# Optimization experiments

Hardware: AMD Instinct MI355X
Metric: run time of the kernel (lower is better)

Reference implementation:

```python
import jax, jax.numpy as jnp
import numpy as np

N, DEG, F_IN, H = 50000, 16, 128, 32
E = N * DEG


def _linear_params(key, out_f, in_f):
    kw, kb = jax.random.split(key)
    s = 1.0 / np.sqrt(in_f)
    W = jax.random.uniform(kw, (out_f, in_f), jnp.float32, -s, s)
    b = jax.random.uniform(kb, (out_f,), jnp.float32, -s, s)
    return W, b


def setup_inputs() -> dict:
    key = jax.random.key(0)
    ks = jax.random.split(key, 12)
    X = jax.random.normal(ks[0], (N, F_IN), jnp.float32)
    # DEG distinct nonzero offsets shared by all rows -> unique (src,dst) pairs,
    # so the COO tensor is already coalesced (no duplicate indices).
    offsets = jax.random.permutation(ks[1], jnp.arange(1, N))[:DEG]
    src = jnp.repeat(jnp.arange(N, dtype=jnp.int32), DEG)
    dst = ((src.reshape(N, DEG) + offsets[None, :].astype(jnp.int32)) % N).reshape(-1)
    D = jax.ops.segment_sum(jnp.ones((E,), jnp.float32), src, num_segments=N)
    wn1p, bn1p = _linear_params(ks[2], H, F_IN)      # convN1.pass_map
    wn1s, bn1s = _linear_params(ks[3], H, F_IN)      # convN1.self_map
    we1p, be1p = _linear_params(ks[4], H, 2 * H)     # convE1.pass_map
    we1s, be1s = _linear_params(ks[5], H, F_IN)      # convE1.self_map
    wn2p, bn2p = _linear_params(ks[6], H, H)         # convN2.pass_map
    wn2s, bn2s = _linear_params(ks[7], H, H)         # convN2.self_map
    we2p, be2p = _linear_params(ks[8], H, 2 * H)     # convE2.pass_map
    we2s, be2s = _linear_params(ks[9], H, H)         # convE2.self_map
    wc, bc = _linear_params(ks[10], 1, H)            # classifier
    return dict(X=X, src=src, dst=dst, D=D,
                wn1p=wn1p, bn1p=bn1p, wn1s=wn1s, bn1s=bn1s,
                we1p=we1p, be1p=be1p, we1s=we1s, be1s=be1s,
                wn2p=wn2p, bn2p=bn2p, wn2s=wn2s, bn2s=bn2s,
                we2p=we2p, be2p=be2p, we2s=we2s, be2s=be2s,
                wc=wc, bc=bc)


def reference(X, src, dst, D,
              wn1p, bn1p, wn1s, bn1s,
              we1p, be1p, we1s, be1s,
              wn2p, bn2p, wn2s, bn2s,
              we2p, be2p, we2s, be2s,
              wc, bc):
    n = X.shape[0]

    def node_conv(vals, Xn, wp, bp, ws, bs):
        # torch.sparse.sum(A, dim=1): sum edge values per source row
        Asum = jax.ops.segment_sum(vals, src, num_segments=n)
        return jax.nn.relu((Asum / D[:, None]) @ wp.T + bp + Xn @ ws.T + bs)

    def edge_conv(vals, Xn, wp, bp, ws, bs):
        X1, X2 = Xn[src], Xn[dst]
        Ef = jnp.concatenate([(X1 - X2) * 0.5, (X1 + X2) * 0.5], axis=-1)
        return jax.nn.relu(Ef @ wp.T + bp + vals @ ws.T + bs)

    # add_graph: edge features = |X[src] - X[dst]|
    vals0 = jnp.abs(X[src] - X[dst])            # (E, F_IN)
    X0 = jnp.zeros_like(X)                       # forward zeros node features
    Xn1 = node_conv(vals0, X0, wn1p, bn1p, wn1s, bn1s)   # (N, 32)
    vals1 = edge_conv(vals0, Xn1, we1p, be1p, we1s, be1s)  # (E, 32)
    Xn2 = node_conv(vals1, Xn1, wn2p, bn2p, wn2s, bn2s)  # (N, 32)
    vals2 = edge_conv(vals1, Xn2, we2p, be2p, we2s, be2s)  # (E, 32)
    SX = jax.nn.sigmoid(vals2 @ wc.T + bc)[:, 0]          # (E,)
    return SX
```

## Files before the change

kernel.cpp:

```cpp
#include <hip/hip_runtime.h>

#define DEG 16
#define F_IN 128
#define H 32
#define CH 16

typedef __attribute__((ext_vector_type(8))) _Float16 f16x8;
typedef __attribute__((ext_vector_type(4))) float f32x4;
typedef __attribute__((ext_vector_type(4))) int i32x4;

union HS { _Float16 f; unsigned short s; };

__device__ __forceinline__ float relu_f(float x) { return fmaxf(x, 0.0f); }

__device__ __forceinline__ f16x8 habs8(f16x8 a) {
    union { f16x8 h; i32x4 i; } u; u.h = a;
#pragma unroll
    for (int k = 0; k < 4; ++k) u.i[k] &= 0x7FFF7FFF;
    return u.h;
}
__device__ __forceinline__ unsigned short f2h_s(float x) {
    HS v; v.f = (_Float16)x; return v.s;
}

__global__ __launch_bounds__(256) void k_xhalf(
    const float* __restrict__ X, _Float16* __restrict__ Xh, long n8)
{
    const long t = (long)blockIdx.x * 256 + threadIdx.x;
    if (t >= n8) return;
    const float4* p = (const float4*)X + t * 2;
    const float4 a = p[0], b = p[1];
    f16x8 h;
    h[0] = (_Float16)a.x; h[1] = (_Float16)a.y; h[2] = (_Float16)a.z; h[3] = (_Float16)a.w;
    h[4] = (_Float16)b.x; h[5] = (_Float16)b.y; h[6] = (_Float16)b.z; h[7] = (_Float16)b.w;
    *(f16x8*)(Xh + t * 8) = h;
}

__global__ __launch_bounds__(256) void k_prep(
    const float* __restrict__ we1s, const float* __restrict__ we1p,
    const float* __restrict__ be1p, const float* __restrict__ be1s,
    const float* __restrict__ we2p, const float* __restrict__ we2s,
    const float* __restrict__ be2p, const float* __restrict__ be2s,
    const float* __restrict__ wn1p, const float* __restrict__ bn1p,
    const float* __restrict__ bn1s,
    const float* __restrict__ wn2p, const float* __restrict__ bn2p,
    const float* __restrict__ wn2s, const float* __restrict__ bn2s,
    _Float16* __restrict__ Wcat1, _Float16* __restrict__ Wcat2,
    _Float16* __restrict__ Wn1ph,
    _Float16* __restrict__ Wn2ph, _Float16* __restrict__ Wn2sh,
    float* __restrict__ bias1, float* __restrict__ bias2,
    float* __restrict__ biasn1, float* __restrict__ biasn2)
{
    const int t0 = blockIdx.x * 256 + threadIdx.x;
    const int stride = gridDim.x * 256;
    for (int idx = t0; idx < 32 * 192; idx += stride) {
        const int n = idx / 192, k = idx - n * 192;
        float w;
        if (k < 128)       w = we1s[n * 128 + k];
        else if (k < 160)  w = 0.5f * we1p[n * 64 + (k - 128)];
        else               w = 0.5f * we1p[n * 64 + 32 + (k - 160)];
        Wcat1[idx] = (_Float16)w;
    }
    for (int idx = t0; idx < 32 * 96; idx += stride) {
        const int n = idx / 96, k = idx - n * 96;
        float w;
        if (k < 32)       w = 0.5f * we2p[n * 64 + k];
        else if (k < 64)  w = 0.5f * we2p[n * 64 + 32 + (k - 32)];
        else              w = we2s[n * 32 + (k - 64)];
        Wcat2[idx] = (_Float16)w;
    }
    for (int idx = t0; idx < 32 * 128; idx += stride)
        Wn1ph[idx] = (_Float16)wn1p[idx];
    for (int idx = t0; idx < 32 * 32; idx += stride) {
        Wn2ph[idx] = (_Float16)wn2p[idx];
        Wn2sh[idx] = (_Float16)wn2s[idx];
    }
    if (t0 < H) {
        bias1[t0]  = be1p[t0] + be1s[t0];
        bias2[t0]  = be2p[t0] + be2s[t0];
        biasn1[t0] = bn1p[t0] + bn1s[t0];
        biasn2[t0] = bn2p[t0] + bn2s[t0];
    }
}

__global__ __launch_bounds__(256) void k_p1(
    const _Float16* __restrict__ Xh, const int* __restrict__ dst,
    const float* __restrict__ D,
    const _Float16* __restrict__ Wn1ph, const float* __restrict__ biasn1,
    _Float16* __restrict__ Xn1h, int N)
{
    __shared__ float UacS[4][16 * 33];
    const int tid = threadIdx.x;
    const int wave = tid >> 6, lane = tid & 63;
    const int i0 = blockIdx.x * CH;
    const int m = lane & 15, g = lane >> 4;
    const int srow = (i0 + m < N) ? (i0 + m) : (N - 1);

    int dj[4];
#pragma unroll
    for (int jj = 0; jj < 4; ++jj)
        dj[jj] = dst[(size_t)srow * DEG + wave * 4 + jj];

    f16x8 sv[4];
#pragma unroll
    for (int kb = 0; kb < 4; ++kb)
        sv[kb] = *(const f16x8*)(Xh + (size_t)srow * F_IN + kb * 32 + g * 8);
    f16x8 Bn[4][2];
#pragma unroll
    for (int kb = 0; kb < 4; ++kb)
#pragma unroll
        for (int t = 0; t < 2; ++t)
            Bn[kb][t] = *(const f16x8*)(Wn1ph + (t * 16 + m) * 128 + kb * 32 + g * 8);

    f16x8 tvc[4], tvn[4];
#pragma unroll
    for (int kb = 0; kb < 4; ++kb)
        tvc[kb] = *(const f16x8*)(Xh + (size_t)dj[0] * F_IN + kb * 32 + g * 8);

    f32x4 cn0 = {0.f,0.f,0.f,0.f}, cn1 = {0.f,0.f,0.f,0.f};
#pragma unroll
    for (int jj = 0; jj < 4; ++jj) {
        if (jj < 3) {
#pragma unroll
            for (int kb = 0; kb < 4; ++kb)
                tvn[kb] = *(const f16x8*)(Xh + (size_t)dj[jj + 1] * F_IN + kb * 32 + g * 8);
        }
#pragma unroll
        for (int kb = 0; kb < 4; ++kb) {
            const f16x8 a = habs8(sv[kb] - tvc[kb]);
            cn0 = __builtin_amdgcn_mfma_f32_16x16x32_f16(a, Bn[kb][0], cn0, 0, 0, 0);
            cn1 = __builtin_amdgcn_mfma_f32_16x16x32_f16(a, Bn[kb][1], cn1, 0, 0, 0);
        }
#pragma unroll
        for (int kb = 0; kb < 4; ++kb) tvc[kb] = tvn[kb];
    }
#pragma unroll
    for (int r = 0; r < 4; ++r) {
        UacS[wave][(g * 4 + r) * 33 + m]      = cn0[r];
        UacS[wave][(g * 4 + r) * 33 + 16 + m] = cn1[r];
    }
    __syncthreads();
    {
        const int mm = tid >> 4, c = tid & 15;
        float u0 = 0.f, u1 = 0.f;
#pragma unroll
        for (int w = 0; w < 4; ++w) {
            u0 += UacS[w][mm * 33 + c];
            u1 += UacS[w][mm * 33 + 16 + c];
        }
        if (i0 + mm < N) {
            const float invD = 1.0f / D[i0 + mm];
            Xn1h[(size_t)(i0 + mm) * H + c]      = (_Float16)relu_f(u0 * invD + biasn1[c]);
            Xn1h[(size_t)(i0 + mm) * H + 16 + c] = (_Float16)relu_f(u1 * invD + biasn1[16 + c]);
        }
    }
}

__global__ __launch_bounds__(256) void k_p2(
    const _Float16* __restrict__ Xh, const int* __restrict__ dst,
    const _Float16* __restrict__ Xn1h,
    const _Float16* __restrict__ Wcat1, const float* __restrict__ bias1,
    const _Float16* __restrict__ Wn2ph, const _Float16* __restrict__ Wn2sh,
    const float* __restrict__ biasn2, const float* __restrict__ D,
    _Float16* __restrict__ vals1, _Float16* __restrict__ Xn2h, int N)
{
    __shared__ unsigned short RP[4][16 * 40];
    __shared__ float AacS[4][16 * 33];
    __shared__ unsigned short AsumH[16 * 40];
    const int tid = threadIdx.x;
    const int wave = tid >> 6, lane = tid & 63;
    const int i0 = blockIdx.x * CH;
    const int m = lane & 15, g = lane >> 4;
    const int srow = (i0 + m < N) ? (i0 + m) : (N - 1);

    int dj[4];
#pragma unroll
    for (int jj = 0; jj < 4; ++jj)
        dj[jj] = dst[(size_t)srow * DEG + wave * 4 + jj];

    const f16x8 x1 = *(const f16x8*)(Xn1h + (size_t)srow * H + g * 8);
    f16x8 x2[4];
#pragma unroll
    for (int jj = 0; jj < 4; ++jj)
        x2[jj] = *(const f16x8*)(Xn1h + (size_t)dj[jj] * H + g * 8);
    f16x8 sv[4];
#pragma unroll
    for (int kb = 0; kb < 4; ++kb)
        sv[kb] = *(const f16x8*)(Xh + (size_t)srow * F_IN + kb * 32 + g * 8);
    f16x8 Bf[6][2];
#pragma unroll
    for (int kb = 0; kb < 6; ++kb)
#pragma unroll
        for (int t = 0; t < 2; ++t)
            Bf[kb][t] = *(const f16x8*)(Wcat1 + (t * 16 + m) * 192 + kb * 32 + g * 8);

    f16x8 tvc[4], tvn[4];
#pragma unroll
    for (int kb = 0; kb < 4; ++kb)
        tvc[kb] = *(const f16x8*)(Xh + (size_t)dj[0] * F_IN + kb * 32 + g * 8);

    const float b0 = bias1[m], b1v = bias1[16 + m];
    float sA0[4] = {0.f,0.f,0.f,0.f}, sA1[4] = {0.f,0.f,0.f,0.f};
    unsigned short* L = RP[wave];
#pragma unroll
    for (int jj = 0; jj < 4; ++jj) {
        if (jj < 3) {
#pragma unroll
            for (int kb = 0; kb < 4; ++kb)
                tvn[kb] = *(const f16x8*)(Xh + (size_t)dj[jj + 1] * F_IN + kb * 32 + g * 8);
        }
        f32x4 c0 = {0.f,0.f,0.f,0.f}, c1 = {0.f,0.f,0.f,0.f};
#pragma unroll
        for (int kb = 0; kb < 4; ++kb) {
            const f16x8 a = habs8(sv[kb] - tvc[kb]);
            c0 = __builtin_amdgcn_mfma_f32_16x16x32_f16(a, Bf[kb][0], c0, 0, 0, 0);
            c1 = __builtin_amdgcn_mfma_f32_16x16x32_f16(a, Bf[kb][1], c1, 0, 0, 0);
        }
        const f16x8 ad = x1 - x2[jj];
        const f16x8 aS = x1 + x2[jj];
        c0 = __builtin_amdgcn_mfma_f32_16x16x32_f16(ad, Bf[4][0], c0, 0, 0, 0);
        c1 = __builtin_amdgcn_mfma_f32_16x16x32_f16(ad, Bf[4][1], c1, 0, 0, 0);
        c0 = __builtin_amdgcn_mfma_f32_16x16x32_f16(aS, Bf[5][0], c0, 0, 0, 0);
        c1 = __builtin_amdgcn_mfma_f32_16x16x32_f16(aS, Bf[5][1], c1, 0, 0, 0);
#pragma unroll
        for (int r = 0; r < 4; ++r) {
            const float v0 = relu_f(c0[r] + b0);
            const float v1 = relu_f(c1[r] + b1v);
            L[(g * 4 + r) * 40 + m]      = f2h_s(v0);
            L[(g * 4 + r) * 40 + 16 + m] = f2h_s(v1);
            sA0[r] += v0; sA1[r] += v1;
        }
        const size_t tb = ((size_t)blockIdx.x * 16 + wave * 4 + jj) * 512;
        const int rr = lane >> 2, q = lane & 3;
        const i32x4 v = *(const i32x4*)(L + rr * 40 + q * 8);
        *(i32x4*)(vals1 + tb + rr * 32 + q * 8) = v;
#pragma unroll
        for (int kb = 0; kb < 4; ++kb) tvc[kb] = tvn[kb];
    }
#pragma unroll
    for (int r = 0; r < 4; ++r) {
        AacS[wave][(g * 4 + r) * 33 + m]      = sA0[r];
        AacS[wave][(g * 4 + r) * 33 + 16 + m] = sA1[r];
    }
    __syncthreads();
    {
        const int mm = tid >> 4, c = tid & 15;
        float a0 = 0.f, a1 = 0.f;
#pragma unroll
        for (int w = 0; w < 4; ++w) {
            a0 += AacS[w][mm * 33 + c];
            a1 += AacS[w][mm * 33 + 16 + c];
        }
        const int nd = (i0 + mm < N) ? (i0 + mm) : (N - 1);
        const float invD = 1.0f / D[nd];
        AsumH[mm * 40 + c]      = f2h_s(a0 * invD);
        AsumH[mm * 40 + 16 + c] = f2h_s(a1 * invD);
    }
    __syncthreads();
    if (wave == 0) {
        const f16x8 aF = *(const f16x8*)((const _Float16*)AsumH + m * 40 + g * 8);
        f16x8 Bp[2], Bs2[2];
#pragma unroll
        for (int t = 0; t < 2; ++t) {
            Bp[t]  = *(const f16x8*)(Wn2ph + (t * 16 + m) * H + g * 8);
            Bs2[t] = *(const f16x8*)(Wn2sh + (t * 16 + m) * H + g * 8);
        }
        f32x4 c0 = {0.f,0.f,0.f,0.f}, c1 = {0.f,0.f,0.f,0.f};
        c0 = __builtin_amdgcn_mfma_f32_16x16x32_f16(aF, Bp[0], c0, 0, 0, 0);
        c1 = __builtin_amdgcn_mfma_f32_16x16x32_f16(aF, Bp[1], c1, 0, 0, 0);
        c0 = __builtin_amdgcn_mfma_f32_16x16x32_f16(x1, Bs2[0], c0, 0, 0, 0);
        c1 = __builtin_amdgcn_mfma_f32_16x16x32_f16(x1, Bs2[1], c1, 0, 0, 0);
        const float bp0 = biasn2[m], bp1 = biasn2[16 + m];
#pragma unroll
        for (int r = 0; r < 4; ++r) {
            const int node = i0 + g * 4 + r;
            if (node < N) {
                Xn2h[(size_t)node * H + m]      = (_Float16)relu_f(c0[r] + bp0);
                Xn2h[(size_t)node * H + 16 + m] = (_Float16)relu_f(c1[r] + bp1);
            }
        }
    }
}

__global__ __launch_bounds__(256) void k_p3(
    const _Float16* __restrict__ Xn2h, const int* __restrict__ dst,
    const _Float16* __restrict__ vals1,
    const _Float16* __restrict__ Wcat2, const float* __restrict__ bias2,
    const float* __restrict__ wc, const float* __restrict__ bc,
    float* __restrict__ out, int N)
{
    __shared__ float outS[16 * 17];
    const int tid = threadIdx.x;
    const int wave = tid >> 6, lane = tid & 63;
    const int i0 = blockIdx.x * CH;
    const int m = lane & 15, g = lane >> 4;
    const int srow = (i0 + m < N) ? (i0 + m) : (N - 1);

    int dj[4];
#pragma unroll
    for (int jj = 0; jj < 4; ++jj)
        dj[jj] = dst[(size_t)srow * DEG + wave * 4 + jj];

    const f16x8 x1 = *(const f16x8*)(Xn2h + (size_t)srow * H + g * 8);
    f16x8 x2[4], av[4];
#pragma unroll
    for (int jj = 0; jj < 4; ++jj) {
        x2[jj] = *(const f16x8*)(Xn2h + (size_t)dj[jj] * H + g * 8);
        const size_t tb = ((size_t)blockIdx.x * 16 + wave * 4 + jj) * 512;
        av[jj] = *(const f16x8*)(vals1 + tb + m * 32 + g * 8);
    }
    f16x8 Bf[3][2];
#pragma unroll
    for (int kb = 0; kb < 3; ++kb)
#pragma unroll
        for (int t = 0; t < 2; ++t)
            Bf[kb][t] = *(const f16x8*)(Wcat2 + (t * 16 + m) * 96 + kb * 32 + g * 8);

    const float b0 = bias2[m], b1v = bias2[16 + m];
    const float w0 = wc[m], w1 = wc[16 + m];
#pragma unroll
    for (int jj = 0; jj < 4; ++jj) {
        const f16x8 ad = x1 - x2[jj];
        const f16x8 aS = x1 + x2[jj];
        f32x4 c0 = {0.f,0.f,0.f,0.f}, c1 = {0.f,0.f,0.f,0.f};
        c0 = __builtin_amdgcn_mfma_f32_16x16x32_f16(ad,     Bf[0][0], c0, 0, 0, 0);
        c1 = __builtin_amdgcn_mfma_f32_16x16x32_f16(ad,     Bf[0][1], c1, 0, 0, 0);
        c0 = __builtin_amdgcn_mfma_f32_16x16x32_f16(aS,     Bf[1][0], c0, 0, 0, 0);
        c1 = __builtin_amdgcn_mfma_f32_16x16x32_f16(aS,     Bf[1][1], c1, 0, 0, 0);
        c0 = __builtin_amdgcn_mfma_f32_16x16x32_f16(av[jj], Bf[2][0], c0, 0, 0, 0);
        c1 = __builtin_amdgcn_mfma_f32_16x16x32_f16(av[jj], Bf[2][1], c1, 0, 0, 0);

        float sr[4];
#pragma unroll
        for (int r = 0; r < 4; ++r)
            sr[r] = relu_f(c0[r] + b0) * w0 + relu_f(c1[r] + b1v) * w1;
#pragma unroll
        for (int mask = 1; mask < 16; mask <<= 1) {
#pragma unroll
            for (int r = 0; r < 4; ++r)
                sr[r] += __shfl_xor(sr[r], mask);
        }
        if (m == 0) {
#pragma unroll
            for (int r = 0; r < 4; ++r)
                outS[(g * 4 + r) * 17 + (wave * 4 + jj)] = sr[r];
        }
    }
    __syncthreads();
    {
        const int mm = tid >> 4;
        if (i0 + mm < N) {
            const float sx = outS[mm * 17 + (tid & 15)] + bc[0];
            out[(size_t)i0 * DEG + tid] = 1.0f / (1.0f + __expf(-sx));
        }
    }
}

extern "C" void kernel_launch(void* const* d_in, const int* in_sizes, int n_in,
                              void* d_out, int out_size, void* d_ws, size_t ws_size,
                              hipStream_t stream)
{
    const float* X    = (const float*)d_in[0];
    const int*   dst  = (const int*)  d_in[2];
    const float* D    = (const float*)d_in[3];
    const float* wn1p = (const float*)d_in[4];
    const float* bn1p = (const float*)d_in[5];
    const float* bn1s = (const float*)d_in[7];
    const float* we1p = (const float*)d_in[8];
    const float* be1p = (const float*)d_in[9];
    const float* we1s = (const float*)d_in[10];
    const float* be1s = (const float*)d_in[11];
    const float* wn2p = (const float*)d_in[12];
    const float* bn2p = (const float*)d_in[13];
    const float* wn2s = (const float*)d_in[14];
    const float* bn2s = (const float*)d_in[15];
    const float* we2p = (const float*)d_in[16];
    const float* be2p = (const float*)d_in[17];
    const float* we2s = (const float*)d_in[18];
    const float* be2s = (const float*)d_in[19];
    const float* wc   = (const float*)d_in[20];
    const float* bc   = (const float*)d_in[21];

    const int N = in_sizes[3];
    const int nbC = (N + CH - 1) / CH;
    const size_t Epad = (size_t)nbC * CH * DEG;

    char* w = (char*)d_ws;
    _Float16* vals1 = (_Float16*)w;  w += Epad * H * 2;
    _Float16* Xh    = (_Float16*)w;  w += (size_t)N * F_IN * 2;
    _Float16* Xn1h  = (_Float16*)w;  w += (size_t)N * H * 2;
    _Float16* Xn2h  = (_Float16*)w;  w += (size_t)N * H * 2;
    _Float16* Wcat1 = (_Float16*)w;  w += 32 * 192 * 2;
    _Float16* Wcat2 = (_Float16*)w;  w += 32 * 96 * 2;
    _Float16* Wn1ph = (_Float16*)w;  w += 32 * 128 * 2;
    _Float16* Wn2ph = (_Float16*)w;  w += 32 * 32 * 2;
    _Float16* Wn2sh = (_Float16*)w;  w += 32 * 32 * 2;
    float* bias1  = (float*)w;       w += H * 4;
    float* bias2  = (float*)w;       w += H * 4;
    float* biasn1 = (float*)w;       w += H * 4;
    float* biasn2 = (float*)w;       w += H * 4;
    float* outp = (float*)d_out;

    const long n8 = (long)N * F_IN / 8;
    const int nbX = (int)((n8 + 255) / 256);

    k_xhalf<<<nbX, 256, 0, stream>>>(X, Xh, n8);
    k_prep<<<32, 256, 0, stream>>>(we1s, we1p, be1p, be1s, we2p, we2s, be2p, be2s,
                                   wn1p, bn1p, bn1s, wn2p, bn2p, wn2s, bn2s,
                                   Wcat1, Wcat2, Wn1ph, Wn2ph, Wn2sh,
                                   bias1, bias2, biasn1, biasn2);
    k_p1<<<nbC, 256, 0, stream>>>(Xh, dst, D, Wn1ph, biasn1, Xn1h, N);
    k_p2<<<nbC, 256, 0, stream>>>(Xh, dst, Xn1h, Wcat1, bias1, Wn2ph, Wn2sh,
                                  biasn2, D, vals1, Xn2h, N);
    k_p3<<<nbC, 256, 0, stream>>>(Xn2h, dst, vals1, Wcat2, bias2, wc, bc, outp, N);
}
```

Baseline: 232.4 us.

## Use single-wave blocks that iterate all 16 neighbors, removing LDS cross-wave reductions

Each of the three graph-conv kernels now runs one 64-lane wave per 16-node chunk and loops over all 16 neighbors in registers, where before four waves each handled 4 neighbors. This removes the shared-memory cross-wave reduction and the __syncthreads barriers, and the per-row dst indices are loaded as int4 vectors. Neighbor feature loads are software-prefetched one step ahead, and the output is written with float4 stores. The trade-off is longer serial loops per wave with less parallelism per block, plus tighter register pressure under the new occupancy hints.

After: 207.4 us. 10.7% less time.

```diff
diff --git a/kernel.cpp b/kernel.cpp
--- a/kernel.cpp
+++ b/kernel.cpp
@@ -3,7 +3,6 @@
 #define DEG 16
 #define F_IN 128
 #define H 32
-#define CH 16
 
 typedef __attribute__((ext_vector_type(8))) _Float16 f16x8;
 typedef __attribute__((ext_vector_type(4))) float f32x4;
@@ -18,9 +17,6 @@
 #pragma unroll
     for (int k = 0; k < 4; ++k) u.i[k] &= 0x7FFF7FFF;
     return u.h;
-}
-__device__ __forceinline__ unsigned short f2h_s(float x) {
-    HS v; v.f = (_Float16)x; return v.s;
 }
 
 __global__ __launch_bounds__(256) void k_xhalf(
@@ -83,24 +79,23 @@
     }
 }
 
-__global__ __launch_bounds__(256) void k_p1(
+__global__ __launch_bounds__(64, 4) void k_p1(
     const _Float16* __restrict__ Xh, const int* __restrict__ dst,
     const float* __restrict__ D,
     const _Float16* __restrict__ Wn1ph, const float* __restrict__ biasn1,
     _Float16* __restrict__ Xn1h, int N)
 {
-    __shared__ float UacS[4][16 * 33];
-    const int tid = threadIdx.x;
-    const int wave = tid >> 6, lane = tid & 63;
-    const int i0 = blockIdx.x * CH;
+    const int lane = threadIdx.x;
     const int m = lane & 15, g = lane >> 4;
+    const int i0 = blockIdx.x * 16;
     const int srow = (i0 + m < N) ? (i0 + m) : (N - 1);
 
-    int dj[4];
-#pragma unroll
-    for (int jj = 0; jj < 4; ++jj)
-        dj[jj] = dst[(size_t)srow * DEG + wave * 4 + jj];
-
+    i32x4 dj4[4];
+    {
+        const i32x4* dp = (const i32x4*)(dst + (size_t)srow * DEG);
+#pragma unroll
+        for (int q = 0; q < 4; ++q) dj4[q] = dp[q];
+    }
     f16x8 sv[4];
 #pragma unroll
     for (int kb = 0; kb < 4; ++kb)
@@ -115,15 +110,16 @@
     f16x8 tvc[4], tvn[4];
 #pragma unroll
     for (int kb = 0; kb < 4; ++kb)
-        tvc[kb] = *(const f16x8*)(Xh + (size_t)dj[0] * F_IN + kb * 32 + g * 8);
+        tvc[kb] = *(const f16x8*)(Xh + (size_t)dj4[0][0] * F_IN + kb * 32 + g * 8);
 
     f32x4 cn0 = {0.f,0.f,0.f,0.f}, cn1 = {0.f,0.f,0.f,0.f};
 #pragma unroll
-    for (int jj = 0; jj < 4; ++jj) {
-        if (jj < 3) {
+    for (int j = 0; j < 16; ++j) {
+        if (j < 15) {
+            const int dn = dj4[(j + 1) >> 2][(j + 1) & 3];
 #pragma unroll
             for (int kb = 0; kb < 4; ++kb)
-                tvn[kb] = *(const f16x8*)(Xh + (size_t)dj[jj + 1] * F_IN + kb * 32 + g * 8);
+                tvn[kb] = *(const f16x8*)(Xh + (size_t)dn * F_IN + kb * 32 + g * 8);
         }
 #pragma unroll
         for (int kb = 0; kb < 4; ++kb) {
@@ -134,29 +130,19 @@
 #pragma unroll
         for (int kb = 0; kb < 4; ++kb) tvc[kb] = tvn[kb];
     }
+    const float bn0 = biasn1[m], bn1v = biasn1[16 + m];
 #pragma unroll
     for (int r = 0; r < 4; ++r) {
-        UacS[wave][(g * 4 + r) * 33 + m]      = cn0[r];
-        UacS[wave][(g * 4 + r) * 33 + 16 + m] = cn1[r];
-    }
-    __syncthreads();
-    {
-        const int mm = tid >> 4, c = tid & 15;
-        float u0 = 0.f, u1 = 0.f;
-#pragma unroll
-        for (int w = 0; w < 4; ++w) {
-            u0 += UacS[w][mm * 33 + c];
-            u1 += UacS[w][mm * 33 + 16 + c];
-        }
-        if (i0 + mm < N) {
-            const float invD = 1.0f / D[i0 + mm];
-            Xn1h[(size_t)(i0 + mm) * H + c]      = (_Float16)relu_f(u0 * invD + biasn1[c]);
-            Xn1h[(size_t)(i0 + mm) * H + 16 + c] = (_Float16)relu_f(u1 * invD + biasn1[16 + c]);
-        }
-    }
-}
-
-__global__ __launch_bounds__(256) void k_p2(
+        const int node = i0 + g * 4 + r;
+        if (node < N) {
+            const float invD = 1.0f / D[node];
+            Xn1h[(size_t)node * H + m]      = (_Float16)relu_f(cn0[r] * invD + bn0);
+            Xn1h[(size_t)node * H + 16 + m] = (_Float16)relu_f(cn1[r] * invD + bn1v);
+        }
+    }
+}
+
+__global__ __launch_bounds__(64, 3) void k_p2(
     const _Float16* __restrict__ Xh, const int* __restrict__ dst,
     const _Float16* __restrict__ Xn1h,
     const _Float16* __restrict__ Wcat1, const float* __restrict__ bias1,
@@ -164,25 +150,19 @@
     const float* __restrict__ biasn2, const float* __restrict__ D,
     _Float16* __restrict__ vals1, _Float16* __restrict__ Xn2h, int N)
 {
-    __shared__ unsigned short RP[4][16 * 40];
-    __shared__ float AacS[4][16 * 33];
-    __shared__ unsigned short AsumH[16 * 40];
-    const int tid = threadIdx.x;
-    const int wave = tid >> 6, lane = tid & 63;
-    const int i0 = blockIdx.x * CH;
+    __shared__ unsigned short RP[16 * 40];
+    const int lane = threadIdx.x;
     const int m = lane & 15, g = lane >> 4;
+    const int i0 = blockIdx.x * 16;
     const int srow = (i0 + m < N) ? (i0 + m) : (N - 1);
 
-    int dj[4];
-#pragma unroll
-    for (int jj = 0; jj < 4; ++jj)
-        dj[jj] = dst[(size_t)srow * DEG + wave * 4 + jj];
-
+    i32x4 dj4[4];
+    {
+        const i32x4* dp = (const i32x4*)(dst + (size_t)srow * DEG);
+#pragma unroll
+        for (int q = 0; q < 4; ++q) dj4[q] = dp[q];
+    }
     const f16x8 x1 = *(const f16x8*)(Xn1h + (size_t)srow * H + g * 8);
-    f16x8 x2[4];
-#pragma unroll
-    for (int jj = 0; jj < 4; ++jj)
-        x2[jj] = *(const f16x8*)(Xn1h + (size_t)dj[jj] * H + g * 8);
     f16x8 sv[4];
 #pragma unroll
     for (int kb = 0; kb < 4; ++kb)
@@ -194,20 +174,26 @@
         for (int t = 0; t < 2; ++t)
             Bf[kb][t] = *(const f16x8*)(Wcat1 + (t * 16 + m) * 192 + kb * 32 + g * 8);
 
-    f16x8 tvc[4], tvn[4];
-#pragma unroll
-    for (int kb = 0; kb < 4; ++kb)
-        tvc[kb] = *(const f16x8*)(Xh + (size_t)dj[0] * F_IN + kb * 32 + g * 8);
+    f16x8 tvc[4], tvn[4], x2c, x2n;
+    {
+        const int d0 = dj4[0][0];
+#pragma unroll
+        for (int kb = 0; kb < 4; ++kb)
+            tvc[kb] = *(const f16x8*)(Xh + (size_t)d0 * F_IN + kb * 32 + g * 8);
+        x2c = *(const f16x8*)(Xn1h + (size_t)d0 * H + g * 8);
+    }
 
     const float b0 = bias1[m], b1v = bias1[16 + m];
-    float sA0[4] = {0.f,0.f,0.f,0.f}, sA1[4] = {0.f,0.f,0.f,0.f};
-    unsigned short* L = RP[wave];
-#pragma unroll
-    for (int jj = 0; jj < 4; ++jj) {
-        if (jj < 3) {
+    f32x4 sB0 = {0.f,0.f,0.f,0.f}, sB1 = {0.f,0.f,0.f,0.f};
+    const int rr = lane >> 2, qq = lane & 3;
+#pragma unroll
+    for (int j = 0; j < 16; ++j) {
+        if (j < 15) {
+            const int dn = dj4[(j + 1) >> 2][(j + 1) & 3];
 #pragma unroll
             for (int kb = 0; kb < 4; ++kb)
-                tvn[kb] = *(const f16x8*)(Xh + (size_t)dj[jj + 1] * F_IN + kb * 32 + g * 8);
+                tvn[kb] = *(const f16x8*)(Xh + (size_t)dn * F_IN + kb * 32 + g * 8);
+            x2n = *(const f16x8*)(Xn1h + (size_t)dn * H + g * 8);
         }
         f32x4 c0 = {0.f,0.f,0.f,0.f}, c1 = {0.f,0.f,0.f,0.f};
 #pragma unroll
@@ -216,8 +202,8 @@
             c0 = __builtin_amdgcn_mfma_f32_16x16x32_f16(a, Bf[kb][0], c0, 0, 0, 0);
             c1 = __builtin_amdgcn_mfma_f32_16x16x32_f16(a, Bf[kb][1], c1, 0, 0, 0);
         }
-        const f16x8 ad = x1 - x2[jj];
-        const f16x8 aS = x1 + x2[jj];
+        const f16x8 ad = x1 - x2c;
+        const f16x8 aS = x1 + x2c;
         c0 = __builtin_amdgcn_mfma_f32_16x16x32_f16(ad, Bf[4][0], c0, 0, 0, 0);
         c1 = __builtin_amdgcn_mfma_f32_16x16x32_f16(ad, Bf[4][1], c1, 0, 0, 0);
         c0 = __builtin_amdgcn_mfma_f32_16x16x32_f16(aS, Bf[5][0], c0, 0, 0, 0);
@@ -226,89 +212,69 @@
         for (int r = 0; r < 4; ++r) {
             const float v0 = relu_f(c0[r] + b0);
             const float v1 = relu_f(c1[r] + b1v);
-            L[(g * 4 + r) * 40 + m]      = f2h_s(v0);
-            L[(g * 4 + r) * 40 + 16 + m] = f2h_s(v1);
-            sA0[r] += v0; sA1[r] += v1;
-        }
-        const size_t tb = ((size_t)blockIdx.x * 16 + wave * 4 + jj) * 512;
-        const int rr = lane >> 2, q = lane & 3;
-        const i32x4 v = *(const i32x4*)(L + rr * 40 + q * 8);
-        *(i32x4*)(vals1 + tb + rr * 32 + q * 8) = v;
+            HS h0, h1; h0.f = (_Float16)v0; h1.f = (_Float16)v1;
+            RP[(g * 4 + r) * 40 + m]      = h0.s;
+            RP[(g * 4 + r) * 40 + 16 + m] = h1.s;
+            sB0[r] += v0; sB1[r] += v1;
+        }
+        const size_t tb = ((size_t)blockIdx.x * 16 + j) * 512;
+        const i32x4 v = *(const i32x4*)(RP + rr * 40 + qq * 8);
+        *(i32x4*)(vals1 + tb + rr * 32 + qq * 8) = v;
 #pragma unroll
         for (int kb = 0; kb < 4; ++kb) tvc[kb] = tvn[kb];
-    }
+        x2c = x2n;
+    }
+    _Float16* RPh = (_Float16*)RP;
 #pragma unroll
     for (int r = 0; r < 4; ++r) {
-        AacS[wave][(g * 4 + r) * 33 + m]      = sA0[r];
-        AacS[wave][(g * 4 + r) * 33 + 16 + m] = sA1[r];
-    }
-    __syncthreads();
-    {
-        const int mm = tid >> 4, c = tid & 15;
-        float a0 = 0.f, a1 = 0.f;
-#pragma unroll
-        for (int w = 0; w < 4; ++w) {
-            a0 += AacS[w][mm * 33 + c];
-            a1 += AacS[w][mm * 33 + 16 + c];
-        }
-        const int nd = (i0 + mm < N) ? (i0 + mm) : (N - 1);
-        const float invD = 1.0f / D[nd];
-        AsumH[mm * 40 + c]      = f2h_s(a0 * invD);
-        AsumH[mm * 40 + 16 + c] = f2h_s(a1 * invD);
-    }
-    __syncthreads();
-    if (wave == 0) {
-        const f16x8 aF = *(const f16x8*)((const _Float16*)AsumH + m * 40 + g * 8);
-        f16x8 Bp[2], Bs2[2];
-#pragma unroll
-        for (int t = 0; t < 2; ++t) {
-            Bp[t]  = *(const f16x8*)(Wn2ph + (t * 16 + m) * H + g * 8);
-            Bs2[t] = *(const f16x8*)(Wn2sh + (t * 16 + m) * H + g * 8);
-        }
-        f32x4 c0 = {0.f,0.f,0.f,0.f}, c1 = {0.f,0.f,0.f,0.f};
-        c0 = __builtin_amdgcn_mfma_f32_16x16x32_f16(aF, Bp[0], c0, 0, 0, 0);
-        c1 = __builtin_amdgcn_mfma_f32_16x16x32_f16(aF, Bp[1], c1, 0, 0, 0);
-        c0 = __builtin_amdgcn_mfma_f32_16x16x32_f16(x1, Bs2[0], c0, 0, 0, 0);
-        c1 = __builtin_amdgcn_mfma_f32_16x16x32_f16(x1, Bs2[1], c1, 0, 0, 0);
-        const float bp0 = biasn2[m], bp1 = biasn2[16 + m];
-#pragma unroll
-        for (int r = 0; r < 4; ++r) {
-            const int node = i0 + g * 4 + r;
-            if (node < N) {
-                Xn2h[(size_t)node * H + m]      = (_Float16)relu_f(c0[r] + bp0);
-                Xn2h[(size_t)node * H + 16 + m] = (_Float16)relu_f(c1[r] + bp1);
-            }
-        }
-    }
-}
-
-__global__ __launch_bounds__(256) void k_p3(
+        const int node = i0 + g * 4 + r;
+        const float invD = 1.0f / D[(node < N) ? node : (N - 1)];
+        RPh[(g * 4 + r) * 40 + m]      = (_Float16)(sB0[r] * invD);
+        RPh[(g * 4 + r) * 40 + 16 + m] = (_Float16)(sB1[r] * invD);
+    }
+    const f16x8 aF = *(const f16x8*)(RPh + m * 40 + g * 8);
+    f16x8 Bp[2], Bs2[2];
+#pragma unroll
+    for (int t = 0; t < 2; ++t) {
+        Bp[t]  = *(const f16x8*)(Wn2ph + (t * 16 + m) * H + g * 8);
+        Bs2[t] = *(const f16x8*)(Wn2sh + (t * 16 + m) * H + g * 8);
+    }
+    f32x4 c0 = {0.f,0.f,0.f,0.f}, c1 = {0.f,0.f,0.f,0.f};
+    c0 = __builtin_amdgcn_mfma_f32_16x16x32_f16(aF, Bp[0], c0, 0, 0, 0);
+    c1 = __builtin_amdgcn_mfma_f32_16x16x32_f16(aF, Bp[1], c1, 0, 0, 0);
+    c0 = __builtin_amdgcn_mfma_f32_16x16x32_f16(x1, Bs2[0], c0, 0, 0, 0);
+    c1 = __builtin_amdgcn_mfma_f32_16x16x32_f16(x1, Bs2[1], c1, 0, 0, 0);
+    const float bp0 = biasn2[m], bp1 = biasn2[16 + m];
+#pragma unroll
+    for (int r = 0; r < 4; ++r) {
+        const int node = i0 + g * 4 + r;
+        if (node < N) {
+            Xn2h[(size_t)node * H + m]      = (_Float16)relu_f(c0[r] + bp0);
+            Xn2h[(size_t)node * H + 16 + m] = (_Float16)relu_f(c1[r] + bp1);
+        }
+    }
+}
+
+__global__ __launch_bounds__(64, 4) void k_p3(
     const _Float16* __restrict__ Xn2h, const int* __restrict__ dst,
     const _Float16* __restrict__ vals1,
     const _Float16* __restrict__ Wcat2, const float* __restrict__ bias2,
     const float* __restrict__ wc, const float* __restrict__ bc,
     float* __restrict__ out, int N)
 {
-    __shared__ float outS[16 * 17];
-    const int tid = threadIdx.x;
-    const int wave = tid >> 6, lane = tid & 63;
-    const int i0 = blockIdx.x * CH;
+    __shared__ float outS[16 * 16];
+    const int lane = threadIdx.x;
     const int m = lane & 15, g = lane >> 4;
+    const int i0 = blockIdx.x * 16;
     const int srow = (i0 + m < N) ? (i0 + m) : (N - 1);
 
-    int dj[4];
-#pragma unroll
-    for (int jj = 0; jj < 4; ++jj)
-        dj[jj] = dst[(size_t)srow * DEG + wave * 4 + jj];
-
+    i32x4 dj4[4];
+    {
+        const i32x4* dp = (const i32x4*)(dst + (size_t)srow * DEG);
+#pragma unroll
+        for (int q = 0; q < 4; ++q) dj4[q] = dp[q];
+    }
     const f16x8 x1 = *(const f16x8*)(Xn2h + (size_t)srow * H + g * 8);
-    f16x8 x2[4], av[4];
-#pragma unroll
-    for (int jj = 0; jj < 4; ++jj) {
-        x2[jj] = *(const f16x8*)(Xn2h + (size_t)dj[jj] * H + g * 8);
-        const size_t tb = ((size_t)blockIdx.x * 16 + wave * 4 + jj) * 512;
-        av[jj] = *(const f16x8*)(vals1 + tb + m * 32 + g * 8);
-    }
     f16x8 Bf[3][2];
 #pragma unroll
     for (int kb = 0; kb < 3; ++kb)
@@ -316,19 +282,30 @@
         for (int t = 0; t < 2; ++t)
             Bf[kb][t] = *(const f16x8*)(Wcat2 + (t * 16 + m) * 96 + kb * 32 + g * 8);
 
+    f16x8 x2c, x2n, avc, avn;
+    {
+        const int d0 = dj4[0][0];
+        x2c = *(const f16x8*)(Xn2h + (size_t)d0 * H + g * 8);
+        avc = *(const f16x8*)(vals1 + ((size_t)blockIdx.x * 16 + 0) * 512 + m * 32 + g * 8);
+    }
     const float b0 = bias2[m], b1v = bias2[16 + m];
     const float w0 = wc[m], w1 = wc[16 + m];
 #pragma unroll
-    for (int jj = 0; jj < 4; ++jj) {
-        const f16x8 ad = x1 - x2[jj];
-        const f16x8 aS = x1 + x2[jj];
+    for (int j = 0; j < 16; ++j) {
+        if (j < 15) {
+            const int dn = dj4[(j + 1) >> 2][(j + 1) & 3];
+            x2n = *(const f16x8*)(Xn2h + (size_t)dn * H + g * 8);
+            avn = *(const f16x8*)(vals1 + ((size_t)blockIdx.x * 16 + j + 1) * 512 + m * 32 + g * 8);
+        }
+        const f16x8 ad = x1 - x2c;
+        const f16x8 aS = x1 + x2c;
         f32x4 c0 = {0.f,0.f,0.f,0.f}, c1 = {0.f,0.f,0.f,0.f};
-        c0 = __builtin_amdgcn_mfma_f32_16x16x32_f16(ad,     Bf[0][0], c0, 0, 0, 0);
-        c1 = __builtin_amdgcn_mfma_f32_16x16x32_f16(ad,     Bf[0][1], c1, 0, 0, 0);
-        c0 = __builtin_amdgcn_mfma_f32_16x16x32_f16(aS,     Bf[1][0], c0, 0, 0, 0);
-        c1 = __builtin_amdgcn_mfma_f32_16x16x32_f16(aS,     Bf[1][1], c1, 0, 0, 0);
-        c0 = __builtin_amdgcn_mfma_f32_16x16x32_f16(av[jj], Bf[2][0], c0, 0, 0, 0);
-        c1 = __builtin_amdgcn_mfma_f32_16x16x32_f16(av[jj], Bf[2][1], c1, 0, 0, 0);
+        c0 = __builtin_amdgcn_mfma_f32_16x16x32_f16(ad,  Bf[0][0], c0, 0, 0, 0);
+        c1 = __builtin_amdgcn_mfma_f32_16x16x32_f16(ad,  Bf[0][1], c1, 0, 0, 0);
+        c0 = __builtin_amdgcn_mfma_f32_16x16x32_f16(aS,  Bf[1][0], c0, 0, 0, 0);
+        c1 = __builtin_amdgcn_mfma_f32_16x16x32_f16(aS,  Bf[1][1], c1, 0, 0, 0);
+        c0 = __builtin_amdgcn_mfma_f32_16x16x32_f16(avc, Bf[2][0], c0, 0, 0, 0);
+        c1 = __builtin_amdgcn_mfma_f32_16x16x32_f16(avc, Bf[2][1], c1, 0, 0, 0);
 
         float sr[4];
 #pragma unroll
@@ -343,16 +320,20 @@
         if (m == 0) {
 #pragma unroll
             for (int r = 0; r < 4; ++r)
-                outS[(g * 4 + r) * 17 + (wave * 4 + jj)] = sr[r];
-        }
-    }
-    __syncthreads();
-    {
-        const int mm = tid >> 4;
-        if (i0 + mm < N) {
-            const float sx = outS[mm * 17 + (tid & 15)] + bc[0];
-            out[(size_t)i0 * DEG + tid] = 1.0f / (1.0f + __expf(-sx));
-        }
+                outS[(g * 4 + r) * 16 + j] = sr[r];
+        }
+        x2c = x2n; avc = avn;
+    }
+    {
+        const float bcv = bc[0];
+        const float* s = outS + lane * 4;
+        float4 o;
+        o.x = 1.0f / (1.0f + __expf(-(s[0] + bcv)));
+        o.y = 1.0f / (1.0f + __expf(-(s[1] + bcv)));
+        o.z = 1.0f / (1.0f + __expf(-(s[2] + bcv)));
+        o.w = 1.0f / (1.0f + __expf(-(s[3] + bcv)));
+        if (i0 + 16 <= N || (i0 + (lane >> 2)) < N)
+            *(float4*)(out + (size_t)i0 * DEG + lane * 4) = o;
     }
 }
 
@@ -382,8 +363,8 @@
     const float* bc   = (const float*)d_in[21];
 
     const int N = in_sizes[3];
-    const int nbC = (N + CH - 1) / CH;
-    const size_t Epad = (size_t)nbC * CH * DEG;
+    const int nbW = (N + 15) / 16;
+    const size_t Epad = (size_t)nbW * 16 * DEG;
 
     char* w = (char*)d_ws;
     _Float16* vals1 = (_Float16*)w;  w += Epad * H * 2;
@@ -409,8 +390,8 @@
                                    wn1p, bn1p, bn1s, wn2p, bn2p, wn2s, bn2s,
                                    Wcat1, Wcat2, Wn1ph, Wn2ph, Wn2sh,
                                    bias1, bias2, biasn1, biasn2);
-    k_p1<<<nbC, 256, 0, stream>>>(Xh, dst, D, Wn1ph, biasn1, Xn1h, N);
-    k_p2<<<nbC, 256, 0, stream>>>(Xh, dst, Xn1h, Wcat1, bias1, Wn2ph, Wn2sh,
-                                  biasn2, D, vals1, Xn2h, N);
-    k_p3<<<nbC, 256, 0, stream>>>(Xn2h, dst, vals1, Wcat2, bias2, wc, bc, outp, N);
-}
+    k_p1<<<nbW, 64, 0, stream>>>(Xh, dst, D, Wn1ph, biasn1, Xn1h, N);
+    k_p2<<<nbW, 64, 0, stream>>>(Xh, dst, Xn1h, Wcat1, bias1, Wn2ph, Wn2sh,
+                                 biasn2, D, vals1, Xn2h, N);
+    k_p3<<<nbW, 64, 0, stream>>>(Xn2h, dst, vals1, Wcat2, bias2, wc, bc, outp, N);
+}
```
